# Kernel tuning notes

Hardware: AMD Instinct MI355X
Metric: run time of the kernel (lower is better)

## Reference

```python
import jax, jax.numpy as jnp
import numpy as np

T = 20.0          # logit temperature self.t
THRESH = 1.0      # self.threshold
D = 768
N_OBJ = 8
N_FRAMES = 5
N_ARGS = 3


def l2norm(x, axis):
    # F.normalize: x / max(||x||_2, eps)
    n = jnp.sqrt(jnp.sum(x * x, axis=axis, keepdims=True))
    return x / jnp.maximum(n, 1e-12)


def ce(logits, labels):
    # nn.CrossEntropyLoss / F.cross_entropy with mean reduction
    ls = jax.nn.log_softmax(logits, axis=-1)
    return -jnp.take_along_axis(ls, labels[:, None], axis=1).mean()


def setup_inputs() -> dict:
    key = jax.random.key(0)
    k1, k2, k3, k4 = jax.random.split(key, 4)
    B, C = 256, 504
    return {
        "obj_feat": jax.random.normal(k1, (B, N_FRAMES, N_OBJ, D), dtype=jnp.float32),
        "text_feature": jax.random.normal(k2, (B, N_FRAMES, 4, D), dtype=jnp.float32),
        "mdl_preds": jax.random.normal(k3, (B, N_FRAMES, C), dtype=jnp.float32),
        "label_tensor": jax.random.randint(k4, (B, N_FRAMES), 0, C, dtype=jnp.int64),
    }


def reference(obj_feat, text_feature, mdl_preds, label_tensor):
    B = text_feature.shape[0]
    NB = N_FRAMES * B  # 5B rows

    # ---- LossB: verb cross entropy over flattened first two dims ----
    C = mdl_preds.shape[-1]
    loss_v = ce(mdl_preds.reshape(NB, C), label_tensor.reshape(NB))

    # ---- normalize features along feature dim ----
    obj = l2norm(obj_feat, axis=3)                     # [B,5,8,768]
    txt = l2norm(text_feature, axis=3)                 # [B,5,4,768]

    obj_flat = obj.reshape(N_OBJ * NB, D)              # [40B,768]
    # args = text slots {0,2,3}
    arg = jnp.concatenate([txt[:, :, 0:1, :], txt[:, :, 2:, :]], axis=2).reshape(-1, D)  # [15B,768]

    logits = (arg @ obj_flat.T) * T                    # [15B,40B]
    logits4 = logits.reshape(NB, N_ARGS, NB, N_OBJ)
    max_value = logits4.max(axis=3)                    # [5B,3,5B]
    max_indices = logits4.argmax(axis=3)               # [5B,3,5B]

    # labels[i*3+j] = argmax over own objects + i*8
    diag_idx = jnp.diagonal(max_indices, axis1=0, axis2=2).T   # [5B,3]
    row = jnp.arange(NB)
    labels_wpg = (diag_idx + (row[:, None] << 3)).reshape(-1)  # [15B]
    loss_wpg = ce(logits.reshape(N_ARGS * NB, N_OBJ * NB), labels_wpg)

    # eye-mask tricks == take the diagonal over (row, candidate-video) axes
    mask = jnp.diagonal(max_value, axis1=0, axis2=2).T > THRESH  # [5B,3] bool
    midx = diag_idx                                              # [5B,3]

    arg3 = arg.reshape(NB, N_ARGS, D)
    txt4 = txt.reshape(NB, 4, D)
    maskf = mask.astype(arg3.dtype)[..., None]
    te = (arg3 * maskf).sum(axis=1) + txt4[:, 1, :]              # [5B,768]

    obj3 = obj_flat.reshape(NB, N_OBJ, D)
    gathered = jnp.take_along_axis(obj3, midx[..., None], axis=1)  # [5B,3,768]
    ve = (gathered * maskf).sum(axis=1)                            # [5B,768]

    te = l2norm(te, axis=1)
    ve = l2norm(ve, axis=1)
    logits_ec = (te @ ve.T) * T                                   # [5B,5B]
    lbl = jnp.arange(NB)
    loss_ec = 0.5 * (ce(logits_ec, lbl) + ce(logits_ec.T, lbl))

    return loss_wpg * 0.3 + loss_v * 0.2 + loss_ec * 0.5
```

## Files before the change

### kernel.cpp

```cpp
#include <hip/hip_runtime.h>
#include <hip/hip_bf16.h>
#include <cstdint>
#include <cstddef>

#define DD 768
#define TSCALE 20.0f

typedef short bf16x8 __attribute__((ext_vector_type(8)));
typedef float f32x4 __attribute__((ext_vector_type(4)));
typedef int   i32x4 __attribute__((ext_vector_type(4)));

__device__ inline float wsum(float v){
  #pragma unroll
  for (int m = 1; m < 64; m <<= 1) v += __shfl_xor(v, m, 64);
  return v;
}
__device__ inline float wmax(float v){
  #pragma unroll
  for (int m = 1; m < 64; m <<= 1) v = fmaxf(v, __shfl_xor(v, m, 64));
  return v;
}

__device__ inline void gload_lds16(const void* g, void* l){
  __builtin_amdgcn_global_load_lds(
      (const __attribute__((address_space(1))) uint32_t*)g,
      (__attribute__((address_space(3))) uint32_t*)l, 16, 0, 0);
}

__device__ inline void store_bf16x4(__hip_bfloat16* p, float4 x){
  __hip_bfloat16 t[4] = {__float2bfloat16(x.x), __float2bfloat16(x.y),
                         __float2bfloat16(x.z), __float2bfloat16(x.w)};
  *(ushort4*)p = *(const ushort4*)t;
}

__device__ inline void store_i8x4(int8_t* p, float4 x){
  int q0 = __float2int_rn(x.x * 127.f), q1 = __float2int_rn(x.y * 127.f);
  int q2 = __float2int_rn(x.z * 127.f), q3 = __float2int_rn(x.w * 127.f);
  uint32_t w = (uint32_t)(uint8_t)(int8_t)q0 | ((uint32_t)(uint8_t)(int8_t)q1 << 8) |
               ((uint32_t)(uint8_t)(int8_t)q2 << 16) | ((uint32_t)(uint8_t)(int8_t)q3 << 24);
  *(uint32_t*)p = w;
}

__global__ __launch_bounds__(256) void diag_teve(
    const float* __restrict__ obj, const float* __restrict__ txt,
    const float* __restrict__ mdl, const int* __restrict__ lab,
    float* __restrict__ diagmax,
    int8_t* __restrict__ obji8, int8_t* __restrict__ argi8,
    __hip_bfloat16* __restrict__ tenb, __hip_bfloat16* __restrict__ venb,
    float* __restrict__ lossv_arr, float* __restrict__ zr, int C)
{
  __shared__ float so[8][DD];
  __shared__ float sa[3][DD];
  __shared__ float st1[DD];
  __shared__ float smask[3];
  __shared__ int   sbi[3];

  const int i = blockIdx.x, tid = threadIdx.x;
  const int lane = tid & 63, w = tid >> 6;
  const float* ob = obj + (size_t)i * 8 * DD;

  if (tid < 5) zr[i * 5 + tid] = 0.f;

  #pragma unroll
  for (int t = 0; t < 2; ++t){
    int k = w * 2 + t;
    float4 v[3]; float ss = 0.f;
    #pragma unroll
    for (int q = 0; q < 3; ++q){
      v[q] = ((const float4*)(ob + k * DD))[lane + q * 64];
      ss += v[q].x * v[q].x + v[q].y * v[q].y + v[q].z * v[q].z + v[q].w * v[q].w;
    }
    ss = wsum(ss);
    float inv = 1.0f / fmaxf(sqrtf(ss), 1e-12f);
    #pragma unroll
    for (int q = 0; q < 3; ++q){
      float4 x = {v[q].x * inv, v[q].y * inv, v[q].z * inv, v[q].w * inv};
      ((float4*)&so[k][0])[lane + q * 64] = x;
      store_i8x4(obji8 + (size_t)(i * 8 + k) * DD + 4 * (lane + q * 64), x);
    }
  }

  float4 a[3];
  {
    int s4 = (w == 0) ? 0 : ((w < 3) ? (w + 1) : 1);
    const float* ap = txt + ((size_t)i * 4 + s4) * DD;
    float ss = 0.f;
    #pragma unroll
    for (int q = 0; q < 3; ++q){
      a[q] = ((const float4*)ap)[lane + q * 64];
      ss += a[q].x * a[q].x + a[q].y * a[q].y + a[q].z * a[q].z + a[q].w * a[q].w;
    }
    ss = wsum(ss);
    float inv = 1.0f / fmaxf(sqrtf(ss), 1e-12f);
    #pragma unroll
    for (int q = 0; q < 3; ++q){
      a[q].x *= inv; a[q].y *= inv; a[q].z *= inv; a[q].w *= inv;
    }
    if (w < 3){
      #pragma unroll
      for (int q = 0; q < 3; ++q){
        ((float4*)&sa[w][0])[lane + q * 64] = a[q];
        store_i8x4(argi8 + (size_t)(i * 3 + w) * DD + 4 * (lane + q * 64), a[q]);
      }
    } else {
      #pragma unroll
      for (int q = 0; q < 3; ++q) ((float4*)st1)[lane + q * 64] = a[q];
    }
  }
  __syncthreads();

  if (w < 3){
    float best = -3.0e38f; int bi = 0;
    for (int k = 0; k < 8; ++k){
      float s = 0.f;
      #pragma unroll
      for (int q = 0; q < 3; ++q){
        float4 v = ((const float4*)&so[k][0])[lane + q * 64];
        s += a[q].x * v.x + a[q].y * v.y + a[q].z * v.z + a[q].w * v.w;
      }
      s = wsum(s);
      if (s > best){ best = s; bi = k; }
    }
    float dm = best * TSCALE;
    if (lane == 0){
      diagmax[i * 3 + w] = dm;
      smask[w] = (dm > 1.0f) ? 1.0f : 0.0f;
      sbi[w] = bi;
    }
  }
  __syncthreads();

  if (w == 0){
    float m0 = smask[0], m1 = smask[1], m2 = smask[2];
    float4 te[3]; float ss = 0.f;
    #pragma unroll
    for (int q = 0; q < 3; ++q){
      float4 t1v = ((const float4*)st1)[lane + q * 64];
      float4 a0 = ((const float4*)&sa[0][0])[lane + q * 64];
      float4 a1 = ((const float4*)&sa[1][0])[lane + q * 64];
      float4 a2 = ((const float4*)&sa[2][0])[lane + q * 64];
      float4 t;
      t.x = ((t1v.x + m0 * a0.x) + m1 * a1.x) + m2 * a2.x;
      t.y = ((t1v.y + m0 * a0.y) + m1 * a1.y) + m2 * a2.y;
      t.z = ((t1v.z + m0 * a0.z) + m1 * a1.z) + m2 * a2.z;
      t.w = ((t1v.w + m0 * a0.w) + m1 * a1.w) + m2 * a2.w;
      te[q] = t;
      ss += t.x * t.x + t.y * t.y + t.z * t.z + t.w * t.w;
    }
    ss = wsum(ss);
    float inv = 1.0f / fmaxf(sqrtf(ss), 1e-12f);
    #pragma unroll
    for (int q = 0; q < 3; ++q){
      float4 x = {te[q].x * inv, te[q].y * inv, te[q].z * inv, te[q].w * inv};
      store_bf16x4(tenb + (size_t)i * DD + lane * 4 + q * 256, x);
    }
  } else if (w == 1){
    float m0 = smask[0], m1 = smask[1], m2 = smask[2];
    int b0 = sbi[0], b1 = sbi[1], b2 = sbi[2];
    float4 ve[3]; float ss = 0.f;
    #pragma unroll
    for (int q = 0; q < 3; ++q){
      float4 w0 = ((const float4*)&so[b0][0])[lane + q * 64];
      float4 w1 = ((const float4*)&so[b1][0])[lane + q * 64];
      float4 w2 = ((const float4*)&so[b2][0])[lane + q * 64];
      float4 t;
      t.x = ((m0 * w0.x + m1 * w1.x)) + m2 * w2.x;
      t.y = ((m0 * w0.y + m1 * w1.y)) + m2 * w2.y;
      t.z = ((m0 * w0.z + m1 * w1.z)) + m2 * w2.z;
      t.w = ((m0 * w0.w + m1 * w1.w)) + m2 * w2.w;
      ve[q] = t;
      ss += t.x * t.x + t.y * t.y + t.z * t.z + t.w * t.w;
    }
    ss = wsum(ss);
    float inv = 1.0f / fmaxf(sqrtf(ss), 1e-12f);
    #pragma unroll
    for (int q = 0; q < 3; ++q){
      float4 x = {ve[q].x * inv, ve[q].y * inv, ve[q].z * inv, ve[q].w * inv};
      store_bf16x4(venb + (size_t)i * DD + lane * 4 + q * 256, x);
    }
  } else if (w == 3){
    const float* x = mdl + (size_t)i * C;
    float mx = -3.0e38f;
    for (int c = lane; c < C; c += 64) mx = fmaxf(mx, x[c]);
    mx = wmax(mx);
    float s = 0.f;
    for (int c = lane; c < C; c += 64) s += expf(x[c] - mx);
    s = wsum(s);
    if (lane == 0) lossv_arr[i] = logf(s) + mx - x[lab[i]];
  }
}

#define MFMAI8(d, av, bv) d = __builtin_amdgcn_mfma_i32_16x16x64_i8(av, bv, d, 0, 0, 0)

__global__ __launch_bounds__(256, 3) void gemms_fused(
    const int8_t* __restrict__ A, const int8_t* __restrict__ B,
    float* __restrict__ sumexp,
    const __hip_bfloat16* __restrict__ ten, const __hip_bfloat16* __restrict__ ven,
    float* __restrict__ rowsum, float* __restrict__ colsum, float* __restrict__ Ldiag,
    int nec, int necx)
{
  __shared__ char lds[49152];
  const int tid = threadIdx.x;
  const int lane = tid & 63, wid = tid >> 6;

  if ((int)blockIdx.x < nec){
    const int bx = blockIdx.x % necx, by = blockIdx.x / necx;
    __hip_bfloat16* As = (__hip_bfloat16*)lds;
    __hip_bfloat16* Bs = (__hip_bfloat16*)(lds + 8192);
    char* AsB = lds; char* BsB = lds + 8192;
    const int wr = wid >> 1, wc = wid & 1;
    f32x4 acc[4][4];
    #pragma unroll
    for (int i2 = 0; i2 < 4; ++i2)
      #pragma unroll
      for (int j = 0; j < 4; ++j) acc[i2][j] = (f32x4){0.f, 0.f, 0.f, 0.f};
    const char* Ab = (const char*)(ten + (size_t)(by * 128) * DD);
    const char* Bb = (const char*)(ven + (size_t)(bx * 128) * DD);
    const int srow = tid >> 2, scol = (tid & 3) * 16;
    const int r = lane & 15, kg = (lane >> 4) * 8;

    for (int kb = 0; kb < DD * 2; kb += 64){
      gload_lds16(Ab + (size_t)srow * (DD*2) + kb + scol, AsB + tid * 16);
      gload_lds16(Ab + (size_t)(srow + 64) * (DD*2) + kb + scol, AsB + 4096 + tid * 16);
      gload_lds16(Bb + (size_t)srow * (DD*2) + kb + scol, BsB + tid * 16);
      gload_lds16(Bb + (size_t)(srow + 64) * (DD*2) + kb + scol, BsB + 4096 + tid * 16);
      __syncthreads();
      bf16x8 af[4], bfr[4];
      #pragma unroll
      for (int mi = 0; mi < 4; ++mi)
        af[mi] = *(const bf16x8*)&As[(wr * 64 + mi * 16 + r) * 32 + kg];
      #pragma unroll
      for (int ni = 0; ni < 4; ++ni)
        bfr[ni] = *(const bf16x8*)&Bs[(wc * 64 + ni * 16 + r) * 32 + kg];
      #pragma unroll
      for (int mi = 0; mi < 4; ++mi)
        #pragma unroll
        for (int ni = 0; ni < 4; ++ni)
          acc[mi][ni] = __builtin_amdgcn_mfma_f32_16x16x32_bf16(af[mi], bfr[ni], acc[mi][ni], 0, 0, 0);
      __syncthreads();
    }
    int rowbase = by * 128 + wr * 64 + ((lane >> 4) << 2);
    float colacc[4] = {0.f, 0.f, 0.f, 0.f};
    #pragma unroll
    for (int mi = 0; mi < 4; ++mi){
      #pragma unroll
      for (int rr = 0; rr < 4; ++rr){
        float s = 0.f;
        #pragma unroll
        for (int ni = 0; ni < 4; ++ni){
          float e = expf(fmaf(acc[mi][ni][rr], TSCALE, -TSCALE));
          s += e; colacc[ni] += e;
        }
        s += __shfl_xor(s, 1, 64); s += __shfl_xor(s, 2, 64);
        s += __shfl_xor(s, 4, 64); s += __shfl_xor(s, 8, 64);
        if ((lane & 15) == 0) atomicAdd(&rowsum[rowbase + mi * 16 + rr], s);
      }
    }
    #pragma unroll
    for (int ni = 0; ni < 4; ++ni){
      float c = colacc[ni];
      c += __shfl_xor(c, 16, 64); c += __shfl_xor(c, 32, 64);
      if (lane < 16) atomicAdd(&colsum[bx * 128 + wc * 64 + ni * 16 + lane], c);
    }
    if (bx == by){
      #pragma unroll
      for (int mi = 0; mi < 4; ++mi)
        #pragma unroll
        for (int ni = 0; ni < 4; ++ni)
          #pragma unroll
          for (int rr = 0; rr < 4; ++rr){
            int grow = wr * 64 + mi * 16 + ((lane >> 4) << 2) + rr;
            int gcol = wc * 64 + ni * 16 + (lane & 15);
            if (grow == gcol) Ldiag[by * 128 + grow] = acc[mi][ni][rr] * TSCALE;
          }
    }
    return;
  }

  const int wr = wid >> 1, wc = wid & 1;
  const int r = lane & 15, kg = lane >> 4;

  int g = blockIdx.x - nec;
  int bx = (g & 7) * 10 + (g >> 3) % 10;
  int by = (g >> 3) / 10;

  const int8_t* Abase = A + (size_t)by * 128 * DD;
  const int8_t* Bbase = B + (size_t)bx * 128 * DD;

  const int srow = tid >> 2, sc = tid & 3;
  const int ssw = ((sc ^ ((srow >> 1) & 3)) * 16);

  auto STAGE = [&](int p, int kt){
    gload_lds16(Abase + (size_t)srow * DD + kt * 64 + ssw, lds + p * 16384 + tid * 16);
    gload_lds16(Abase + (size_t)(64 + srow) * DD + kt * 64 + ssw, lds + p * 16384 + 4096 + tid * 16);
    gload_lds16(Bbase + (size_t)srow * DD + kt * 64 + ssw, lds + p * 16384 + 8192 + tid * 16);
    gload_lds16(Bbase + (size_t)(64 + srow) * DD + kt * 64 + ssw, lds + p * 16384 + 12288 + tid * 16);
  };
  auto LDA = [&](int p, int mi)->i32x4 {
    int row = wr * 64 + mi * 16 + r;
    return *(const i32x4*)(lds + p * 16384 + row * 64 + ((kg ^ ((row >> 1) & 3)) * 16));
  };
  auto LDB = [&](int p, int ni)->i32x4 {
    int row = wc * 64 + ni * 16 + r;
    return *(const i32x4*)(lds + p * 16384 + 8192 + row * 64 + ((kg ^ ((row >> 1) & 3)) * 16));
  };

  i32x4 acc[4][4];
  #pragma unroll
  for (int mi = 0; mi < 4; ++mi)
    #pragma unroll
    for (int ni = 0; ni < 4; ++ni) acc[mi][ni] = (i32x4){0, 0, 0, 0};

  STAGE(0, 0); STAGE(1, 1);
  #pragma unroll
  for (int t = 0; t < 12; ++t){
    if (t < 11) asm volatile("s_waitcnt vmcnt(4)" ::: "memory");
    else        asm volatile("s_waitcnt vmcnt(0)" ::: "memory");
    __builtin_amdgcn_s_barrier();
    __builtin_amdgcn_sched_barrier(0);
    if (t < 10) STAGE((t + 2) % 3, t + 2);
    const int p = t % 3;
    i32x4 af[4], bf[4];
    #pragma unroll
    for (int mi = 0; mi < 4; ++mi) af[mi] = LDA(p, mi);
    #pragma unroll
    for (int ni = 0; ni < 4; ++ni) bf[ni] = LDB(p, ni);
    __builtin_amdgcn_s_setprio(1);
    #pragma unroll
    for (int mi = 0; mi < 4; ++mi)
      #pragma unroll
      for (int ni = 0; ni < 4; ++ni) MFMAI8(acc[mi][ni], af[mi], bf[ni]);
    __builtin_amdgcn_s_setprio(0);
  }

  const float SC = TSCALE / 16129.0f;
  const int rowbase = by * 128 + wr * 64 + kg * 4;
  #pragma unroll
  for (int mi = 0; mi < 4; ++mi){
    #pragma unroll
    for (int rr = 0; rr < 4; ++rr){
      float s = 0.f;
      #pragma unroll
      for (int ni = 0; ni < 4; ++ni) s += expf(fmaf((float)acc[mi][ni][rr], SC, -TSCALE));
      s += __shfl_xor(s, 1, 64); s += __shfl_xor(s, 2, 64);
      s += __shfl_xor(s, 4, 64); s += __shfl_xor(s, 8, 64);
      if (r == 0) atomicAdd(&sumexp[rowbase + mi * 16 + rr], s);
    }
  }
}

__global__ __launch_bounds__(256) void finalize_kernel(
    const float* __restrict__ sumexp, const float* __restrict__ diagmax,
    const float* __restrict__ rowsum, const float* __restrict__ colsum,
    const float* __restrict__ Ldiag, const float* __restrict__ lossv_arr,
    float* __restrict__ out, int NB)
{
  int tid = threadIdx.x;
  float p = 0.f;
  for (int r = tid; r < 3 * NB; r += 256) p += logf(sumexp[r]) + TSCALE - diagmax[r];
  p *= (0.3f / (3.0f * NB));
  float q = 0.f, lv = 0.f;
  for (int i2 = tid; i2 < NB; i2 += 256){
    q += (logf(rowsum[i2]) + TSCALE - Ldiag[i2]) + (logf(colsum[i2]) + TSCALE - Ldiag[i2]);
    lv += lossv_arr[i2];
  }
  p += q * (0.25f / NB) + lv * (0.2f / NB);
  __shared__ float red[256];
  red[tid] = p; __syncthreads();
  for (int s = 128; s > 0; s >>= 1){ if (tid < s) red[tid] += red[tid + s]; __syncthreads(); }
  if (tid == 0) out[0] = red[0];
}

extern "C" void kernel_launch(void* const* d_in, const int* in_sizes, int n_in,
                              void* d_out, int out_size, void* d_ws, size_t ws_size,
                              hipStream_t stream) {
  const float* obj = (const float*)d_in[0];
  const float* txt = (const float*)d_in[1];
  const float* mdl = (const float*)d_in[2];
  const int*   lab = (const int*)d_in[3];

  const int NB = in_sizes[1] / (4 * DD);
  const int C  = in_sizes[2] / NB;

  float* ws = (float*)d_ws;
  size_t o = 0;
  int8_t* obji8 = (int8_t*)(ws + o); o += (size_t)NB * 8 * DD / 4;
  int8_t* argi8 = (int8_t*)(ws + o); o += (size_t)NB * 3 * DD / 4;
  __hip_bfloat16* tenb = (__hip_bfloat16*)(ws + o); o += (size_t)NB * DD / 2;
  __hip_bfloat16* venb = (__hip_bfloat16*)(ws + o); o += (size_t)NB * DD / 2;
  float* diagmax = ws + o; o += (size_t)3 * NB;
  float* Ldiag = ws + o; o += (size_t)NB;
  float* lossv_arr = ws + o; o += (size_t)NB;
  float* zr = ws + o;
  float* sumexp = zr;
  float* rowsum = zr + 3 * NB;
  float* colsum = rowsum + NB;

  diag_teve<<<NB, 256, 0, stream>>>(obj, txt, mdl, lab, diagmax, obji8, argi8,
                                    tenb, venb, lossv_arr, zr, C);
  const int necx = NB / 128;
  const int nec = necx * necx;
  const int nwpg = (NB * 3 / 128) * (NB * 8 / 128);
  gemms_fused<<<nec + nwpg, 256, 0, stream>>>(argi8, obji8, sumexp, tenb, venb,
                                              rowsum, colsum, Ldiag, nec, necx);
  finalize_kernel<<<1, 256, 0, stream>>>(sumexp, diagmax, rowsum, colsum, Ldiag, lossv_arr,
                                         (float*)d_out, NB);
}
```

Before: 107.4 us.

## Retile int8 logit GEMM to 64x256 with full-K A panel in LDS

The int8 argument-by-object GEMM changes from 128x128 tiles to 64x256 tiles. The whole 64-row A panel across the full K dimension is loaded into LDS once. Each wave streams its own 64-column B slab through a private double buffer, so the per-iteration block barriers go away. This is meant to cut A reloads and synchronisation, at the cost of more LDS per block (80 KB) and lower occupancy (launch bounds drop to 2 blocks), with a hardcoded grid mapping.

```diff
diff --git a/kernel.cpp b/kernel.cpp
--- a/kernel.cpp
+++ b/kernel.cpp
@@ -192,14 +192,14 @@
 
 #define MFMAI8(d, av, bv) d = __builtin_amdgcn_mfma_i32_16x16x64_i8(av, bv, d, 0, 0, 0)
 
-__global__ __launch_bounds__(256, 3) void gemms_fused(
+__global__ __launch_bounds__(256, 2) void gemms_fused(
     const int8_t* __restrict__ A, const int8_t* __restrict__ B,
     float* __restrict__ sumexp,
     const __hip_bfloat16* __restrict__ ten, const __hip_bfloat16* __restrict__ ven,
     float* __restrict__ rowsum, float* __restrict__ colsum, float* __restrict__ Ldiag,
     int nec, int necx)
 {
-  __shared__ char lds[49152];
+  __shared__ char lds[81920];
   const int tid = threadIdx.x;
   const int lane = tid & 63, wid = tid >> 6;
 
@@ -277,32 +277,44 @@
     return;
   }
 
-  const int wr = wid >> 1, wc = wid & 1;
   const int r = lane & 15, kg = lane >> 4;
 
   int g = blockIdx.x - nec;
-  int bx = (g & 7) * 10 + (g >> 3) % 10;
-  int by = (g >> 3) / 10;
-
-  const int8_t* Abase = A + (size_t)by * 128 * DD;
-  const int8_t* Bbase = B + (size_t)bx * 128 * DD;
-
-  const int srow = tid >> 2, sc = tid & 3;
-  const int ssw = ((sc ^ ((srow >> 1) & 3)) * 16);
-
-  auto STAGE = [&](int p, int kt){
-    gload_lds16(Abase + (size_t)srow * DD + kt * 64 + ssw, lds + p * 16384 + tid * 16);
-    gload_lds16(Abase + (size_t)(64 + srow) * DD + kt * 64 + ssw, lds + p * 16384 + 4096 + tid * 16);
-    gload_lds16(Bbase + (size_t)srow * DD + kt * 64 + ssw, lds + p * 16384 + 8192 + tid * 16);
-    gload_lds16(Bbase + (size_t)(64 + srow) * DD + kt * 64 + ssw, lds + p * 16384 + 12288 + tid * 16);
+  int bx = (g & 7) * 5 + (g >> 3) % 5;
+  int by = (g >> 3) / 5;
+
+  const int8_t* Abase = A + (size_t)by * 64 * DD;
+  const int8_t* Bbase = B + ((size_t)bx * 256 + (size_t)wid * 64) * DD;
+  char* Apan = lds;
+  char* Bbuf = lds + 49152 + wid * 8192;
+
+  #pragma unroll
+  for (int j = 0; j < 12; ++j){
+    int c = j * 256 + tid;
+    int row = c / 48, cc = c - row * 48;
+    int cc2 = (cc & ~7) | ((cc & 7) ^ (row & 7));
+    gload_lds16(Abase + (size_t)row * DD + cc2 * 16, Apan + c * 16);
+  }
+
+  auto STAGE_B = [&](int p, int kt){
+    #pragma unroll
+    for (int j = 0; j < 4; ++j){
+      int c = j * 64 + lane;
+      int row = c >> 2, cc = c & 3;
+      int cc2 = cc ^ ((row >> 1) & 3);
+      gload_lds16(Bbase + (size_t)row * DD + kt * 64 + cc2 * 16,
+                  Bbuf + p * 4096 + c * 16);
+    }
   };
-  auto LDA = [&](int p, int mi)->i32x4 {
-    int row = wr * 64 + mi * 16 + r;
-    return *(const i32x4*)(lds + p * 16384 + row * 64 + ((kg ^ ((row >> 1) & 3)) * 16));
+  auto LDA = [&](int mi, int t)->i32x4 {
+    int row = mi * 16 + r;
+    int ch = t * 4 + kg;
+    int chs = (ch & ~7) | ((ch & 7) ^ (row & 7));
+    return *(const i32x4*)(Apan + row * 768 + chs * 16);
   };
   auto LDB = [&](int p, int ni)->i32x4 {
-    int row = wc * 64 + ni * 16 + r;
-    return *(const i32x4*)(lds + p * 16384 + 8192 + row * 64 + ((kg ^ ((row >> 1) & 3)) * 16));
+    int row = ni * 16 + r;
+    return *(const i32x4*)(Bbuf + p * 4096 + row * 64 + ((kg ^ ((row >> 1) & 3)) * 16));
   };
 
   i32x4 acc[4][4];
@@ -311,20 +323,22 @@
     #pragma unroll
     for (int ni = 0; ni < 4; ++ni) acc[mi][ni] = (i32x4){0, 0, 0, 0};
 
-  STAGE(0, 0); STAGE(1, 1);
+  STAGE_B(0, 0); STAGE_B(1, 1);
+  __syncthreads();
+
   #pragma unroll
   for (int t = 0; t < 12; ++t){
-    if (t < 11) asm volatile("s_waitcnt vmcnt(4)" ::: "memory");
-    else        asm volatile("s_waitcnt vmcnt(0)" ::: "memory");
-    __builtin_amdgcn_s_barrier();
+    if (t >= 2 && t < 11) asm volatile("s_waitcnt vmcnt(4)" ::: "memory");
+    else if (t == 11)     asm volatile("s_waitcnt vmcnt(0)" ::: "memory");
+    const int p = t & 1;
+    i32x4 af[4], bf[4];
+    #pragma unroll
+    for (int mi = 0; mi < 4; ++mi) af[mi] = LDA(mi, t);
+    #pragma unroll
+    for (int ni = 0; ni < 4; ++ni) bf[ni] = LDB(p, ni);
+    asm volatile("s_waitcnt lgkmcnt(0)" ::: "memory");
     __builtin_amdgcn_sched_barrier(0);
-    if (t < 10) STAGE((t + 2) % 3, t + 2);
-    const int p = t % 3;
-    i32x4 af[4], bf[4];
-    #pragma unroll
-    for (int mi = 0; mi < 4; ++mi) af[mi] = LDA(p, mi);
-    #pragma unroll
-    for (int ni = 0; ni < 4; ++ni) bf[ni] = LDB(p, ni);
+    if (t < 10) STAGE_B(p, t + 2);
     __builtin_amdgcn_s_setprio(1);
     #pragma unroll
     for (int mi = 0; mi < 4; ++mi)
@@ -334,7 +348,7 @@
   }
 
   const float SC = TSCALE / 16129.0f;
-  const int rowbase = by * 128 + wr * 64 + kg * 4;
+  const int rowbase = by * 64 + kg * 4;
   #pragma unroll
   for (int mi = 0; mi < 4; ++mi){
     #pragma unroll
@@ -400,7 +414,7 @@
                                     tenb, venb, lossv_arr, zr, C);
   const int necx = NB / 128;
   const int nec = necx * necx;
-  const int nwpg = (NB * 3 / 128) * (NB * 8 / 128);
+  const int nwpg = (NB * 3 / 64) * (NB * 8 / 256);
   gemms_fused<<<nec + nwpg, 256, 0, stream>>>(argi8, obji8, sumexp, tenb, venb,
                                               rowsum, colsum, Ldiag, nec, necx);
   finalize_kernel<<<1, 256, 0, stream>>>(sumexp, diagmax, rowsum, colsum, Ldiag, lossv_arr,
```

Result: slower. 135.8 us (+26.5%).
